# Optimization experiments

Measured on AMD Instinct MI355X. Metric: run time of the kernel, lower is better.

## Reference

```python
import jax, jax.numpy as jnp
import numpy as np

N_STATE = 1024
N_HEAD = 16
D_K = N_STATE // N_HEAD  # 64


def setup_inputs() -> dict:
    key = jax.random.key(0)
    ks = jax.random.split(key, 12)
    B, S = 2, 2048
    s = 1.0 / np.sqrt(N_STATE)
    inp = {
        "q": jax.random.normal(ks[0], (B, S, N_STATE), jnp.float32),
        "k": jax.random.normal(ks[1], (B, S, N_STATE), jnp.float32),
        "v": jax.random.normal(ks[2], (B, S, N_STATE), jnp.float32),
        # Linear weights in torch layout [out_features, in_features]
        "Wq": jax.random.normal(ks[3], (N_STATE, N_STATE), jnp.float32) * s,
        "bq": jax.random.normal(ks[4], (N_STATE,), jnp.float32) * s,
        "Wk": jax.random.normal(ks[5], (N_STATE, N_STATE), jnp.float32) * s,
        "bk": jax.random.normal(ks[6], (N_STATE,), jnp.float32) * s,
        "Wv": jax.random.normal(ks[7], (N_STATE, N_STATE), jnp.float32) * s,
        "bv": jax.random.normal(ks[8], (N_STATE,), jnp.float32) * s,
        "Wo": jax.random.normal(ks[9], (N_STATE, N_STATE), jnp.float32) * s,
        "bo": jax.random.normal(ks[10], (N_STATE,), jnp.float32) * s,
    }
    return inp


def reference(q, k, v, Wq, bq, Wk, bk, Wv, bv, Wo, bo):
    B = q.shape[0]
    # projections (torch Linear: x @ W.T + b), split heads -> [B, H, S, d]
    def proj(x, W, b):
        y = jnp.einsum('bsi,oi->bso', x, W) + b
        return y.reshape(B, -1, N_HEAD, D_K).transpose(0, 2, 1, 3)
    qh = proj(q, Wq, bq)
    kh = proj(k, Wk, bk)
    vh = proj(v, Wv, bv)
    # scaled dot-product attention, full [B,H,Sq,Sk] scores as in original
    scores = jnp.einsum('bhqd,bhkd->bhqk', qh, kh) / np.sqrt(D_K).astype(np.float32)
    attn = jax.nn.softmax(scores, axis=-1)
    out = jnp.einsum('bhqk,bhkd->bhqd', attn, vh)
    out = out.transpose(0, 2, 1, 3).reshape(B, -1, N_HEAD * D_K)
    return jnp.einsum('bsi,oi->bso', out, Wo) + bo
```

## Files before the change

kernel.cpp:

```cpp
#include <hip/hip_runtime.h>
#include <stdint.h>

typedef __attribute__((ext_vector_type(8))) short short8;
typedef __attribute__((ext_vector_type(4))) float f32x4;
typedef __attribute__((ext_vector_type(4))) uint32_t u32x4;

#if __has_builtin(__builtin_amdgcn_exp2f)
#define EXP2(x) __builtin_amdgcn_exp2f(x)
#else
#define EXP2(x) exp2f(x)
#endif

__device__ __forceinline__ short f2bf(float f){
  uint32_t u = __builtin_bit_cast(uint32_t, f);
  return (short)((u + 0x8000u) >> 16);
}
__device__ __forceinline__ uint32_t pk2(float lo, float hi){
  uint32_t a = __builtin_bit_cast(uint32_t, lo) + 0x8000u;
  uint32_t b = __builtin_bit_cast(uint32_t, hi) + 0x8000u;
#if __has_builtin(__builtin_amdgcn_perm)
  return __builtin_amdgcn_perm(b, a, 0x07060302u);
#else
  return (b & 0xFFFF0000u) | (a >> 16);
#endif
}
__device__ __forceinline__ void gload16(const void* g, void* l){
  __builtin_amdgcn_global_load_lds((const __attribute__((address_space(1))) void*)g,
                                   (__attribute__((address_space(3))) void*)l, 16, 0, 0);
}

__global__ __launch_bounds__(512) void cvt_all(
    const float* __restrict__ q, const float* __restrict__ k, const float* __restrict__ v,
    const float* __restrict__ wq, const float* __restrict__ wk, const float* __restrict__ wv,
    const float* __restrict__ wo, short* __restrict__ dst){
  const size_t SQ = 4096ull*1024ull, NW = 1024ull*1024ull;
  size_t e = (size_t)(blockIdx.x*512u + threadIdx.x)*8ull;
  const float* src; size_t rel;
  if (e < 3*SQ){ size_t which = e / SQ; src = which==0?q:(which==1?k:v); rel = e - which*SQ; }
  else { size_t e2 = e - 3*SQ; size_t which = e2 / NW;
         src = which==0?wq:(which==1?wk:(which==2?wv:wo)); rel = e2 - which*NW; }
  float4 a = *(const float4*)(src + rel);
  float4 b = *(const float4*)(src + rel + 4);
  u32x4 r = { pk2(a.x,a.y), pk2(a.z,a.w), pk2(b.x,b.y), pk2(b.z,b.w) };
  *(u32x4*)(dst + e) = r;
}

template<int MODE>
__device__ __forceinline__ void gemm_body(const short* __restrict__ A, const short* __restrict__ Bw,
    const float* __restrict__ bias, void* __restrict__ Cout, float scale, int m0, int n0){
  const int K = 1024;
  __shared__ short Al[128*64];
  __shared__ short Bl[64*64];
  int tid = threadIdx.x;
  int w = tid >> 6, lane = tid & 63, lr = lane & 15, lg = lane >> 4;
  int wr = w >> 1, wc = w & 1;
  f32x4 acc[2][2] = {};
  int row0 = tid >> 3;
  int qc0  = (tid & 7) ^ (row0 & 7);
  const short* Ag = A  + (size_t)(m0 + row0)*K + qc0*8;
  const short* Bg = Bw + (size_t)(n0 + row0)*K + qc0*8;
  char* Alb = (char*)Al + tid*16;
  char* Blb = (char*)Bl + tid*16;
  int ra[2], rb[2];
#pragma unroll
  for (int mi=0; mi<2; ++mi){ int r = wr*32 + mi*16 + lr; ra[mi] = r; }
#pragma unroll
  for (int ni=0; ni<2; ++ni){ int r = wc*32 + ni*16 + lr; rb[ni] = r; }
  for (int k0 = 0; k0 < K; k0 += 64){
    gload16(Ag + k0,                Alb);
    gload16(Ag + k0 + 64*(size_t)K, Alb + 8192);
    gload16(Bg + k0,                Blb);
    __syncthreads();
#pragma unroll
    for (int kk=0; kk<2; ++kk){
      short8 av[2], bv[2];
#pragma unroll
      for (int mi=0; mi<2; ++mi)
        av[mi] = *(const short8*)((char*)Al + ra[mi]*128 + (((kk*4 + lg) ^ (ra[mi] & 7)) << 4));
#pragma unroll
      for (int ni=0; ni<2; ++ni)
        bv[ni] = *(const short8*)((char*)Bl + rb[ni]*128 + (((kk*4 + lg) ^ (rb[ni] & 7)) << 4));
#pragma unroll
      for (int mi=0; mi<2; ++mi)
#pragma unroll
        for (int ni=0; ni<2; ++ni)
          acc[mi][ni] = __builtin_amdgcn_mfma_f32_16x16x32_bf16(av[mi], bv[ni], acc[mi][ni], 0, 0, 0);
    }
    __syncthreads();
  }
#pragma unroll
  for (int ni=0; ni<2; ++ni){
    int col = n0 + wc*32 + ni*16 + lr;
    float bb = bias[col];
#pragma unroll
    for (int mi=0; mi<2; ++mi){
#pragma unroll
      for (int i2=0; i2<4; ++i2){
        int row = m0 + wr*32 + mi*16 + lg*4 + i2;
        float val = (acc[mi][ni][i2] + bb) * scale;
        if (MODE == 0){
          int b = row >> 11, s = row & 2047, h = col >> 6, d = col & 63;
          ((short*)Cout)[(((size_t)(b*16 + h))*2048 + s)*64 + d] = f2bf(val);
        } else {
          ((float*)Cout)[(size_t)row*1024 + col] = val;
        }
      }
    }
  }
}

__global__ __launch_bounds__(512) void gemm_qkv(
    const short* __restrict__ qb, const short* __restrict__ kb, const short* __restrict__ vb,
    const short* __restrict__ Wqb, const short* __restrict__ Wkb, const short* __restrict__ Wvb,
    const float* __restrict__ bq, const float* __restrict__ bk, const float* __restrict__ bv,
    short* __restrict__ Qh, short* __restrict__ Kh, short* __restrict__ Vh, float qscale){
  int f = (blockIdx.z*32 + blockIdx.y)*16 + blockIdx.x;
  int L = (f & 7)*192 + (f >> 3);
  int z = L >> 9, r = L & 511;
  int m0 = (r >> 4)*128, n0 = (r & 15)*64;
  const short* A  = z==0 ? qb  : (z==1 ? kb  : vb);
  const short* Bw = z==0 ? Wqb : (z==1 ? Wkb : Wvb);
  const float* bi = z==0 ? bq  : (z==1 ? bk  : bv);
  short* C        = z==0 ? Qh  : (z==1 ? Kh  : Vh);
  float s = z==0 ? qscale : 1.0f;
  gemm_body<0>(A, Bw, bi, (void*)C, s, m0, n0);
}

__global__ __launch_bounds__(512) void gemm_out(const short* __restrict__ A, const short* __restrict__ Bw,
    const float* __restrict__ bias, float* __restrict__ Cout){
  int f = blockIdx.y*gridDim.x + blockIdx.x;
  int L = (f & 7)*64 + (f >> 3);
  int m0 = (L >> 4)*128, n0 = (L & 15)*64;
  gemm_body<1>(A, Bw, bias, (void*)Cout, 1.0f, m0, n0);
}

__global__ __launch_bounds__(512) void attn_fwd(const short* __restrict__ Qh, const short* __restrict__ Kh,
    const short* __restrict__ Vh, short* __restrict__ AO){
  const int S = 2048;
  int i = blockIdx.y*gridDim.x + blockIdx.x;
  int L = (i & 7)*64 + (i >> 3);
  int bh = L >> 4, qt = L & 15;
  __shared__ short Kl[3][4096];
  __shared__ short Vt[2][64*72];
  int tid = threadIdx.x, w = tid >> 6, lane = tid & 63, lr = lane & 15, lg = lane >> 4;
  const short* Qb = Qh + (size_t)bh*S*64;
  const short* Kb = Kh + (size_t)bh*S*64;
  const short* Vb = Vh + (size_t)bh*S*64;
  int q0 = qt*128 + w*16;
  short8 aq[2];
#pragma unroll
  for (int h=0; h<2; ++h)
    aq[h] = *(const short8*)&Qb[(size_t)(q0 + lr)*64 + h*32 + lg*8];
  f32x4 o[4] = {};
  float lsum = 0.f;
  int koff = tid*16;
  int kr = tid >> 3, kc = tid & 7;
  int ksw = (kr & 3) | (((kr >> 3) & 1) << 2);
  int ksrc = kr*64 + ((kc ^ ksw) << 3);
  int Rbase = 8*(lr >> 2) + (lr & 3);
  int sR = (lr & 3) | (((lr >> 2) & 1) << 2);
  int slot0 = (lg ^ sR) << 3, slot1 = ((lg + 4) ^ sR) << 3;
  int vr = tid >> 3;
  int d0 = (tid & 7)*8;
  int c0 = vr ^ d0;
  gload16(Kb + ksrc,        (char*)&Kl[0][0] + koff);
  gload16(Kb + 4096 + ksrc, (char*)&Kl[1][0] + koff);
  {
    short8 v0 = *(const short8*)&Vb[(size_t)vr*64 + d0];
#pragma unroll
    for (int j=0; j<8; ++j) Vt[0][(d0 + j)*72 + c0] = v0[j];
  }
  asm volatile("s_waitcnt vmcnt(1) lgkmcnt(0)" ::: "memory");
  __builtin_amdgcn_sched_barrier(0);
  __builtin_amdgcn_s_barrier();

  for (int t = 0; t < 32; ++t){
    int buf = t % 3;
    short8 nv;
    if (t + 1 < 32)
      nv = *(const short8*)&Vb[(size_t)((t + 1)*64 + vr)*64 + d0];
    if (t + 2 < 32)
      gload16(Kb + (size_t)(t + 2)*4096 + ksrc, (char*)&Kl[(t + 2) % 3][0] + koff);
    const short* Kbuf = &Kl[buf][0];
    uint32_t Wp[2][2][2];
    __builtin_amdgcn_s_setprio(1);
#pragma unroll
    for (int nf=0; nf<4; ++nf){
      int R = Rbase + (nf & 1)*4 + (nf >> 1)*32;
      short8 ak0 = *(const short8*)&Kbuf[R*64 + slot0];
      short8 ak1 = *(const short8*)&Kbuf[R*64 + slot1];
      f32x4 z = {};
      z = __builtin_amdgcn_mfma_f32_16x16x32_bf16(ak0, aq[0], z, 0, 0, 0);
      z = __builtin_amdgcn_mfma_f32_16x16x32_bf16(ak1, aq[1], z, 0, 0, 0);
      float p0 = EXP2(z[0]), p1 = EXP2(z[1]);
      float p2 = EXP2(z[2]), p3 = EXP2(z[3]);
      lsum += (p0 + p1) + (p2 + p3);
      Wp[nf >> 1][nf & 1][0] = pk2(p0, p1);
      Wp[nf >> 1][nf & 1][1] = pk2(p2, p3);
    }
    __builtin_amdgcn_s_setprio(0);
    short8 pa[2];
#pragma unroll
    for (int c=0; c<2; ++c){
      union { uint32_t u[4]; short8 s; } tt;
      tt.u[0] = Wp[c][0][0]; tt.u[1] = Wp[c][0][1];
      tt.u[2] = Wp[c][1][0]; tt.u[3] = Wp[c][1][1];
      pa[c] = tt.s;
    }
    const short* Vbuf = &Vt[t & 1][0];
    __builtin_amdgcn_s_setprio(1);
#pragma unroll
    for (int df=0; df<4; ++df){
      int h = (df*2 + (lr >> 3)) & 7;
      int rowv = (df*16 + lr)*72;
      short8 vb0 = *(const short8*)&Vbuf[rowv + ((lg ^ h) << 3)];
      short8 vb1 = *(const short8*)&Vbuf[rowv + (((lg + 4) ^ h) << 3)];
      o[df] = __builtin_amdgcn_mfma_f32_16x16x32_bf16(pa[0], vb0, o[df], 0, 0, 0);
      o[df] = __builtin_amdgcn_mfma_f32_16x16x32_bf16(pa[1], vb1, o[df], 0, 0, 0);
    }
    __builtin_amdgcn_s_setprio(0);
    if (t + 1 < 32){
      short* Vn = &Vt[(t + 1) & 1][0];
#pragma unroll
      for (int j=0; j<8; ++j) Vn[(d0 + j)*72 + c0] = nv[j];
      if (t < 30) asm volatile("s_waitcnt vmcnt(1) lgkmcnt(0)" ::: "memory");
      else        asm volatile("s_waitcnt vmcnt(0) lgkmcnt(0)" ::: "memory");
      __builtin_amdgcn_sched_barrier(0);
      __builtin_amdgcn_s_barrier();
    }
  }
  lsum += __shfl_xor(lsum, 16); lsum += __shfl_xor(lsum, 32);
  int b = bh >> 4, hh = bh & 15;
  float rinv[4];
#pragma unroll
  for (int i2=0; i2<4; ++i2) rinv[i2] = 1.0f / __shfl(lsum, (lg << 2) + i2);
#pragma unroll
  for (int df=0; df<4; ++df)
#pragma unroll
    for (int i2=0; i2<4; ++i2){
      int row = q0 + lg*4 + i2;
      int col = df*16 + lr;
      AO[((size_t)(b*2048 + row))*1024 + hh*64 + col] = f2bf(o[df][i2] * rinv[i2]);
    }
}

extern "C" void kernel_launch(void* const* d_in, const int* in_sizes, int n_in,
                              void* d_out, int out_size, void* d_ws, size_t ws_size,
                              hipStream_t stream){
  const float* q  = (const float*)d_in[0];
  const float* k  = (const float*)d_in[1];
  const float* v  = (const float*)d_in[2];
  const float* Wq = (const float*)d_in[3];
  const float* bq = (const float*)d_in[4];
  const float* Wk = (const float*)d_in[5];
  const float* bk = (const float*)d_in[6];
  const float* Wv = (const float*)d_in[7];
  const float* bv = (const float*)d_in[8];
  const float* Wo = (const float*)d_in[9];
  const float* bo = (const float*)d_in[10];

  const size_t SQ = 4096ull*1024ull, NW = 1024ull*1024ull;
  short* ws  = (short*)d_ws;
  short* qb  = ws;
  short* kb  = ws + SQ;
  short* vb  = ws + 2*SQ;
  short* Wqb = ws + 3*SQ;
  short* Wkb = Wqb + NW;
  short* Wvb = Wkb + NW;
  short* Wob = Wvb + NW;
  short* Qh  = Wob + NW;
  short* Kh  = Qh + SQ;
  short* Vh  = Kh + SQ;
  short* AO  = qb;

  const float Csc = 0.18033688011112042f;

  cvt_all<<<4096, 512, 0, stream>>>(q, k, v, Wq, Wk, Wv, Wo, ws);
  gemm_qkv<<<dim3(16, 32, 3), 512, 0, stream>>>(qb, kb, vb, Wqb, Wkb, Wvb, bq, bk, bv, Qh, Kh, Vh, Csc);
  attn_fwd<<<dim3(16, 32), 512, 0, stream>>>(Qh, Kh, Vh, AO);
  gemm_out<<<dim3(16, 32), 512, 0, stream>>>(AO, Wob, bo, (float*)d_out);
}
```

Measured before the change: 118.6 us.

## Give each attention wave two query tiles and halve block size

The attention kernel now runs 256 threads per block, and each wave handles 32 query rows (two 16-row MFMA tiles) instead of 16. Each K and V fragment read from LDS is therefore used for twice as many MFMAs, and each thread issues two global-to-LDS loads per tile to keep the per-block load volume the same. The aim is to cut LDS read traffic per unit of compute. In exchange, per-thread register use roughly doubles for accumulators and P fragments, and each block has fewer waves to hide latency.

```diff
diff --git a/kernel.cpp b/kernel.cpp
--- a/kernel.cpp
+++ b/kernel.cpp
@@ -134,7 +134,7 @@
   gemm_body<1>(A, Bw, bias, (void*)Cout, 1.0f, m0, n0);
 }
 
-__global__ __launch_bounds__(512) void attn_fwd(const short* __restrict__ Qh, const short* __restrict__ Kh,
+__global__ __launch_bounds__(256) void attn_fwd(const short* __restrict__ Qh, const short* __restrict__ Kh,
     const short* __restrict__ Vh, short* __restrict__ AO){
   const int S = 2048;
   int i = blockIdx.y*gridDim.x + blockIdx.x;
@@ -146,13 +146,15 @@
   const short* Qb = Qh + (size_t)bh*S*64;
   const short* Kb = Kh + (size_t)bh*S*64;
   const short* Vb = Vh + (size_t)bh*S*64;
-  int q0 = qt*128 + w*16;
-  short8 aq[2];
-#pragma unroll
-  for (int h=0; h<2; ++h)
-    aq[h] = *(const short8*)&Qb[(size_t)(q0 + lr)*64 + h*32 + lg*8];
-  f32x4 o[4] = {};
-  float lsum = 0.f;
+  int q0 = qt*128 + w*32;
+  short8 aq[2][2];
+#pragma unroll
+  for (int m=0; m<2; ++m)
+#pragma unroll
+    for (int h=0; h<2; ++h)
+      aq[m][h] = *(const short8*)&Qb[(size_t)(q0 + m*16 + lr)*64 + h*32 + lg*8];
+  f32x4 o[2][4] = {};
+  float lsum[2] = {0.f, 0.f};
   int koff = tid*16;
   int kr = tid >> 3, kc = tid & 7;
   int ksw = (kr & 3) | (((kr >> 3) & 1) << 2);
@@ -162,51 +164,65 @@
   int slot0 = (lg ^ sR) << 3, slot1 = ((lg + 4) ^ sR) << 3;
   int vr = tid >> 3;
   int d0 = (tid & 7)*8;
-  int c0 = vr ^ d0;
-  gload16(Kb + ksrc,        (char*)&Kl[0][0] + koff);
-  gload16(Kb + 4096 + ksrc, (char*)&Kl[1][0] + koff);
+  int c0 = vr ^ d0, c1 = (vr + 32) ^ d0;
+  gload16(Kb + ksrc,               (char*)&Kl[0][0] + koff);
+  gload16(Kb + ksrc + 2048,        (char*)&Kl[0][0] + koff + 4096);
+  gload16(Kb + 4096 + ksrc,        (char*)&Kl[1][0] + koff);
+  gload16(Kb + 4096 + ksrc + 2048, (char*)&Kl[1][0] + koff + 4096);
   {
     short8 v0 = *(const short8*)&Vb[(size_t)vr*64 + d0];
-#pragma unroll
-    for (int j=0; j<8; ++j) Vt[0][(d0 + j)*72 + c0] = v0[j];
-  }
-  asm volatile("s_waitcnt vmcnt(1) lgkmcnt(0)" ::: "memory");
+    short8 v1 = *(const short8*)&Vb[(size_t)(vr + 32)*64 + d0];
+#pragma unroll
+    for (int j=0; j<8; ++j){ Vt[0][(d0 + j)*72 + c0] = v0[j]; Vt[0][(d0 + j)*72 + c1] = v1[j]; }
+  }
+  asm volatile("s_waitcnt vmcnt(2) lgkmcnt(0)" ::: "memory");
   __builtin_amdgcn_sched_barrier(0);
   __builtin_amdgcn_s_barrier();
 
   for (int t = 0; t < 32; ++t){
     int buf = t % 3;
-    short8 nv;
-    if (t + 1 < 32)
-      nv = *(const short8*)&Vb[(size_t)((t + 1)*64 + vr)*64 + d0];
-    if (t + 2 < 32)
-      gload16(Kb + (size_t)(t + 2)*4096 + ksrc, (char*)&Kl[(t + 2) % 3][0] + koff);
+    short8 nv0, nv1;
+    if (t + 1 < 32){
+      nv0 = *(const short8*)&Vb[(size_t)((t + 1)*64 + vr)*64 + d0];
+      nv1 = *(const short8*)&Vb[(size_t)((t + 1)*64 + vr + 32)*64 + d0];
+    }
+    if (t + 2 < 32){
+      const short* Kt = Kb + (size_t)(t + 2)*4096;
+      char* Kd = (char*)&Kl[(t + 2) % 3][0] + koff;
+      gload16(Kt + ksrc,        Kd);
+      gload16(Kt + ksrc + 2048, Kd + 4096);
+    }
     const short* Kbuf = &Kl[buf][0];
-    uint32_t Wp[2][2][2];
+    uint32_t Wp[2][2][2][2];
     __builtin_amdgcn_s_setprio(1);
 #pragma unroll
     for (int nf=0; nf<4; ++nf){
       int R = Rbase + (nf & 1)*4 + (nf >> 1)*32;
       short8 ak0 = *(const short8*)&Kbuf[R*64 + slot0];
       short8 ak1 = *(const short8*)&Kbuf[R*64 + slot1];
-      f32x4 z = {};
-      z = __builtin_amdgcn_mfma_f32_16x16x32_bf16(ak0, aq[0], z, 0, 0, 0);
-      z = __builtin_amdgcn_mfma_f32_16x16x32_bf16(ak1, aq[1], z, 0, 0, 0);
-      float p0 = EXP2(z[0]), p1 = EXP2(z[1]);
-      float p2 = EXP2(z[2]), p3 = EXP2(z[3]);
-      lsum += (p0 + p1) + (p2 + p3);
-      Wp[nf >> 1][nf & 1][0] = pk2(p0, p1);
-      Wp[nf >> 1][nf & 1][1] = pk2(p2, p3);
+#pragma unroll
+      for (int m=0; m<2; ++m){
+        f32x4 z = {};
+        z = __builtin_amdgcn_mfma_f32_16x16x32_bf16(ak0, aq[m][0], z, 0, 0, 0);
+        z = __builtin_amdgcn_mfma_f32_16x16x32_bf16(ak1, aq[m][1], z, 0, 0, 0);
+        float p0 = EXP2(z[0]), p1 = EXP2(z[1]);
+        float p2 = EXP2(z[2]), p3 = EXP2(z[3]);
+        lsum[m] += (p0 + p1) + (p2 + p3);
+        Wp[m][nf >> 1][nf & 1][0] = pk2(p0, p1);
+        Wp[m][nf >> 1][nf & 1][1] = pk2(p2, p3);
+      }
     }
     __builtin_amdgcn_s_setprio(0);
-    short8 pa[2];
-#pragma unroll
-    for (int c=0; c<2; ++c){
-      union { uint32_t u[4]; short8 s; } tt;
-      tt.u[0] = Wp[c][0][0]; tt.u[1] = Wp[c][0][1];
-      tt.u[2] = Wp[c][1][0]; tt.u[3] = Wp[c][1][1];
-      pa[c] = tt.s;
-    }
+    short8 pa[2][2];
+#pragma unroll
+    for (int m=0; m<2; ++m)
+#pragma unroll
+      for (int c=0; c<2; ++c){
+        union { uint32_t u[4]; short8 s; } tt;
+        tt.u[0] = Wp[m][c][0][0]; tt.u[1] = Wp[m][c][0][1];
+        tt.u[2] = Wp[m][c][1][0]; tt.u[3] = Wp[m][c][1][1];
+        pa[m][c] = tt.s;
+      }
     const short* Vbuf = &Vt[t & 1][0];
     __builtin_amdgcn_s_setprio(1);
 #pragma unroll
@@ -215,33 +231,40 @@
       int rowv = (df*16 + lr)*72;
       short8 vb0 = *(const short8*)&Vbuf[rowv + ((lg ^ h) << 3)];
       short8 vb1 = *(const short8*)&Vbuf[rowv + (((lg + 4) ^ h) << 3)];
-      o[df] = __builtin_amdgcn_mfma_f32_16x16x32_bf16(pa[0], vb0, o[df], 0, 0, 0);
-      o[df] = __builtin_amdgcn_mfma_f32_16x16x32_bf16(pa[1], vb1, o[df], 0, 0, 0);
+#pragma unroll
+      for (int m=0; m<2; ++m){
+        o[m][df] = __builtin_amdgcn_mfma_f32_16x16x32_bf16(pa[m][0], vb0, o[m][df], 0, 0, 0);
+        o[m][df] = __builtin_amdgcn_mfma_f32_16x16x32_bf16(pa[m][1], vb1, o[m][df], 0, 0, 0);
+      }
     }
     __builtin_amdgcn_s_setprio(0);
     if (t + 1 < 32){
       short* Vn = &Vt[(t + 1) & 1][0];
 #pragma unroll
-      for (int j=0; j<8; ++j) Vn[(d0 + j)*72 + c0] = nv[j];
-      if (t < 30) asm volatile("s_waitcnt vmcnt(1) lgkmcnt(0)" ::: "memory");
+      for (int j=0; j<8; ++j){ Vn[(d0 + j)*72 + c0] = nv0[j]; Vn[(d0 + j)*72 + c1] = nv1[j]; }
+      if (t < 30) asm volatile("s_waitcnt vmcnt(2) lgkmcnt(0)" ::: "memory");
       else        asm volatile("s_waitcnt vmcnt(0) lgkmcnt(0)" ::: "memory");
       __builtin_amdgcn_sched_barrier(0);
       __builtin_amdgcn_s_barrier();
     }
   }
-  lsum += __shfl_xor(lsum, 16); lsum += __shfl_xor(lsum, 32);
+  lsum[0] += __shfl_xor(lsum[0], 16); lsum[0] += __shfl_xor(lsum[0], 32);
+  lsum[1] += __shfl_xor(lsum[1], 16); lsum[1] += __shfl_xor(lsum[1], 32);
   int b = bh >> 4, hh = bh & 15;
-  float rinv[4];
-#pragma unroll
-  for (int i2=0; i2<4; ++i2) rinv[i2] = 1.0f / __shfl(lsum, (lg << 2) + i2);
-#pragma unroll
-  for (int df=0; df<4; ++df)
-#pragma unroll
-    for (int i2=0; i2<4; ++i2){
-      int row = q0 + lg*4 + i2;
-      int col = df*16 + lr;
-      AO[((size_t)(b*2048 + row))*1024 + hh*64 + col] = f2bf(o[df][i2] * rinv[i2]);
-    }
+#pragma unroll
+  for (int m=0; m<2; ++m){
+    float rinv[4];
+#pragma unroll
+    for (int i2=0; i2<4; ++i2) rinv[i2] = 1.0f / __shfl(lsum[m], (lg << 2) + i2);
+#pragma unroll
+    for (int df=0; df<4; ++df)
+#pragma unroll
+      for (int i2=0; i2<4; ++i2){
+        int row = q0 + m*16 + lg*4 + i2;
+        int col = df*16 + lr;
+        AO[((size_t)(b*2048 + row))*1024 + hh*64 + col] = f2bf(o[m][df][i2] * rinv[i2]);
+      }
+  }
 }
 
 extern "C" void kernel_launch(void* const* d_in, const int* in_sizes, int n_in,
@@ -277,6 +300,6 @@
 
   cvt_all<<<4096, 512, 0, stream>>>(q, k, v, Wq, Wk, Wv, Wo, ws);
   gemm_qkv<<<dim3(16, 32, 3), 512, 0, stream>>>(qb, kb, vb, Wqb, Wkb, Wvb, bq, bk, bv, Qh, Kh, Vh, Csc);
-  attn_fwd<<<dim3(16, 32), 512, 0, stream>>>(Qh, Kh, Vh, AO);
+  attn_fwd<<<dim3(16, 32), 256, 0, stream>>>(Qh, Kh, Vh, AO);
   gemm_out<<<dim3(16, 32), 512, 0, stream>>>(AO, Wob, bo, (float*)d_out);
 }
```

New measurement: 127.5 us. 7.5% more time.

## Write V transposed from projection GEMM and async-load it in attention

Applied to the files above, without the earlier changes.

The V projection epilogue now writes V in a per-head [d, S] transposed layout with packed 4-element bf16 stores. The attention kernel then loads V tiles with the same async global-to-LDS path and triple buffering used for K, dropping the per-thread register load and scalar LDS transpose scatter. This removes eight scalar LDS stores per thread per tile and the lgkmcnt wait on them, at the cost of more LDS for a third V buffer and strided global reads along the 2048-long rows.

```diff
diff --git a/kernel.cpp b/kernel.cpp
--- a/kernel.cpp
+++ b/kernel.cpp
@@ -94,15 +94,24 @@
     float bb = bias[col];
 #pragma unroll
     for (int mi=0; mi<2; ++mi){
-#pragma unroll
-      for (int i2=0; i2<4; ++i2){
-        int row = m0 + wr*32 + mi*16 + lg*4 + i2;
-        float val = (acc[mi][ni][i2] + bb) * scale;
-        if (MODE == 0){
-          int b = row >> 11, s = row & 2047, h = col >> 6, d = col & 63;
-          ((short*)Cout)[(((size_t)(b*16 + h))*2048 + s)*64 + d] = f2bf(val);
-        } else {
-          ((float*)Cout)[(size_t)row*1024 + col] = val;
+      if (MODE == 2){
+        int row = m0 + wr*32 + mi*16 + lg*4;
+        int b = row >> 11, s = row & 2047, h = col >> 6, d = col & 63;
+        uint2 val;
+        val.x = pk2((acc[mi][ni][0] + bb)*scale, (acc[mi][ni][1] + bb)*scale);
+        val.y = pk2((acc[mi][ni][2] + bb)*scale, (acc[mi][ni][3] + bb)*scale);
+        *(uint2*)&((short*)Cout)[(((size_t)(b*16 + h))*64 + d)*2048 + s] = val;
+      } else {
+#pragma unroll
+        for (int i2=0; i2<4; ++i2){
+          int row = m0 + wr*32 + mi*16 + lg*4 + i2;
+          float val = (acc[mi][ni][i2] + bb) * scale;
+          if (MODE == 0){
+            int b = row >> 11, s = row & 2047, h = col >> 6, d = col & 63;
+            ((short*)Cout)[(((size_t)(b*16 + h))*2048 + s)*64 + d] = f2bf(val);
+          } else {
+            ((float*)Cout)[(size_t)row*1024 + col] = val;
+          }
         }
       }
     }
@@ -113,7 +122,7 @@
     const short* __restrict__ qb, const short* __restrict__ kb, const short* __restrict__ vb,
     const short* __restrict__ Wqb, const short* __restrict__ Wkb, const short* __restrict__ Wvb,
     const float* __restrict__ bq, const float* __restrict__ bk, const float* __restrict__ bv,
-    short* __restrict__ Qh, short* __restrict__ Kh, short* __restrict__ Vh, float qscale){
+    short* __restrict__ Qh, short* __restrict__ Kh, short* __restrict__ VhT, float qscale){
   int f = (blockIdx.z*32 + blockIdx.y)*16 + blockIdx.x;
   int L = (f & 7)*192 + (f >> 3);
   int z = L >> 9, r = L & 511;
@@ -121,9 +130,9 @@
   const short* A  = z==0 ? qb  : (z==1 ? kb  : vb);
   const short* Bw = z==0 ? Wqb : (z==1 ? Wkb : Wvb);
   const float* bi = z==0 ? bq  : (z==1 ? bk  : bv);
-  short* C        = z==0 ? Qh  : (z==1 ? Kh  : Vh);
-  float s = z==0 ? qscale : 1.0f;
-  gemm_body<0>(A, Bw, bi, (void*)C, s, m0, n0);
+  short* C        = z==0 ? Qh  : (z==1 ? Kh  : VhT);
+  if (z == 2) gemm_body<2>(A, Bw, bi, (void*)C, 1.0f, m0, n0);
+  else        gemm_body<0>(A, Bw, bi, (void*)C, z==0 ? qscale : 1.0f, m0, n0);
 }
 
 __global__ __launch_bounds__(512) void gemm_out(const short* __restrict__ A, const short* __restrict__ Bw,
@@ -135,17 +144,17 @@
 }
 
 __global__ __launch_bounds__(512) void attn_fwd(const short* __restrict__ Qh, const short* __restrict__ Kh,
-    const short* __restrict__ Vh, short* __restrict__ AO){
+    const short* __restrict__ VhT, short* __restrict__ AO){
   const int S = 2048;
   int i = blockIdx.y*gridDim.x + blockIdx.x;
   int L = (i & 7)*64 + (i >> 3);
   int bh = L >> 4, qt = L & 15;
   __shared__ short Kl[3][4096];
-  __shared__ short Vt[2][64*72];
+  __shared__ short Vl[3][4096];
   int tid = threadIdx.x, w = tid >> 6, lane = tid & 63, lr = lane & 15, lg = lane >> 4;
-  const short* Qb = Qh + (size_t)bh*S*64;
-  const short* Kb = Kh + (size_t)bh*S*64;
-  const short* Vb = Vh + (size_t)bh*S*64;
+  const short* Qb = Qh  + (size_t)bh*S*64;
+  const short* Kb = Kh  + (size_t)bh*S*64;
+  const short* Vb = VhT + (size_t)bh*64*2048;
   int q0 = qt*128 + w*16;
   short8 aq[2];
 #pragma unroll
@@ -157,30 +166,26 @@
   int kr = tid >> 3, kc = tid & 7;
   int ksw = (kr & 3) | (((kr >> 3) & 1) << 2);
   int ksrc = kr*64 + ((kc ^ ksw) << 3);
+  int vsrc = kr*2048 + ((kc ^ (kr & 7)) << 3);
   int Rbase = 8*(lr >> 2) + (lr & 3);
   int sR = (lr & 3) | (((lr >> 2) & 1) << 2);
   int slot0 = (lg ^ sR) << 3, slot1 = ((lg + 4) ^ sR) << 3;
-  int vr = tid >> 3;
-  int d0 = (tid & 7)*8;
-  int c0 = vr ^ d0;
+  int vx = lr & 7;
   gload16(Kb + ksrc,        (char*)&Kl[0][0] + koff);
+  gload16(Vb + vsrc,        (char*)&Vl[0][0] + koff);
   gload16(Kb + 4096 + ksrc, (char*)&Kl[1][0] + koff);
-  {
-    short8 v0 = *(const short8*)&Vb[(size_t)vr*64 + d0];
-#pragma unroll
-    for (int j=0; j<8; ++j) Vt[0][(d0 + j)*72 + c0] = v0[j];
-  }
-  asm volatile("s_waitcnt vmcnt(1) lgkmcnt(0)" ::: "memory");
+  gload16(Vb + vsrc + 64,   (char*)&Vl[1][0] + koff);
+  asm volatile("s_waitcnt vmcnt(2) lgkmcnt(0)" ::: "memory");
   __builtin_amdgcn_sched_barrier(0);
   __builtin_amdgcn_s_barrier();
 
   for (int t = 0; t < 32; ++t){
     int buf = t % 3;
-    short8 nv;
-    if (t + 1 < 32)
-      nv = *(const short8*)&Vb[(size_t)((t + 1)*64 + vr)*64 + d0];
-    if (t + 2 < 32)
-      gload16(Kb + (size_t)(t + 2)*4096 + ksrc, (char*)&Kl[(t + 2) % 3][0] + koff);
+    if (t + 2 < 32){
+      int nb = (t + 2) % 3;
+      gload16(Kb + (size_t)(t + 2)*4096 + ksrc, (char*)&Kl[nb][0] + koff);
+      gload16(Vb + vsrc + (t + 2)*64,           (char*)&Vl[nb][0] + koff);
+    }
     const short* Kbuf = &Kl[buf][0];
     uint32_t Wp[2][2][2];
     __builtin_amdgcn_s_setprio(1);
@@ -207,24 +212,20 @@
       tt.u[2] = Wp[c][1][0]; tt.u[3] = Wp[c][1][1];
       pa[c] = tt.s;
     }
-    const short* Vbuf = &Vt[t & 1][0];
+    const short* Vbuf = &Vl[buf][0];
     __builtin_amdgcn_s_setprio(1);
 #pragma unroll
     for (int df=0; df<4; ++df){
-      int h = (df*2 + (lr >> 3)) & 7;
-      int rowv = (df*16 + lr)*72;
-      short8 vb0 = *(const short8*)&Vbuf[rowv + ((lg ^ h) << 3)];
-      short8 vb1 = *(const short8*)&Vbuf[rowv + (((lg + 4) ^ h) << 3)];
+      int rowv = (df*16 + lr)*64;
+      short8 vb0 = *(const short8*)&Vbuf[rowv + ((lg ^ vx) << 3)];
+      short8 vb1 = *(const short8*)&Vbuf[rowv + (((4 + lg) ^ vx) << 3)];
       o[df] = __builtin_amdgcn_mfma_f32_16x16x32_bf16(pa[0], vb0, o[df], 0, 0, 0);
       o[df] = __builtin_amdgcn_mfma_f32_16x16x32_bf16(pa[1], vb1, o[df], 0, 0, 0);
     }
     __builtin_amdgcn_s_setprio(0);
     if (t + 1 < 32){
-      short* Vn = &Vt[(t + 1) & 1][0];
-#pragma unroll
-      for (int j=0; j<8; ++j) Vn[(d0 + j)*72 + c0] = nv[j];
-      if (t < 30) asm volatile("s_waitcnt vmcnt(1) lgkmcnt(0)" ::: "memory");
-      else        asm volatile("s_waitcnt vmcnt(0) lgkmcnt(0)" ::: "memory");
+      if (t < 30) asm volatile("s_waitcnt vmcnt(2)" ::: "memory");
+      else        asm volatile("s_waitcnt vmcnt(0)" ::: "memory");
       __builtin_amdgcn_sched_barrier(0);
       __builtin_amdgcn_s_barrier();
     }
@@ -270,13 +271,13 @@
   short* Wob = Wvb + NW;
   short* Qh  = Wob + NW;
   short* Kh  = Qh + SQ;
-  short* Vh  = Kh + SQ;
+  short* VhT = Kh + SQ;
   short* AO  = qb;
 
   const float Csc = 0.18033688011112042f;
 
   cvt_all<<<4096, 512, 0, stream>>>(q, k, v, Wq, Wk, Wv, Wo, ws);
-  gemm_qkv<<<dim3(16, 32, 3), 512, 0, stream>>>(qb, kb, vb, Wqb, Wkb, Wvb, bq, bk, bv, Qh, Kh, Vh, Csc);
-  attn_fwd<<<dim3(16, 32), 512, 0, stream>>>(Qh, Kh, Vh, AO);
+  gemm_qkv<<<dim3(16, 32, 3), 512, 0, stream>>>(qb, kb, vb, Wqb, Wkb, Wvb, bq, bk, bv, Qh, Kh, VhT, Csc);
+  attn_fwd<<<dim3(16, 32), 512, 0, stream>>>(Qh, Kh, VhT, AO);
   gemm_out<<<dim3(16, 32), 512, 0, stream>>>(AO, Wob, bo, (float*)d_out);
 }
```

Result: no change. 120.5 us (+1.6%).
